# Kernel optimization log

Hardware: AMD Instinct MI355X
Metric: run time of the kernel (lower is better)

Reference implementation:

```python
import jax, jax.numpy as jnp
import numpy as np

NUM_STEPS = 5  # DVF2DDF(num_steps=5)


def _warp(vol, ddf, mode):
    """MONAI Warp: sample vol at (voxel index + ddf), align_corners=True, zeros padding.
    vol: [N,C,D,H,W]; ddf: [N,3,D,H,W] (channels = d,h,w displacement)."""
    N, C, D, H, W = vol.shape
    gd, gh, gw = jnp.meshgrid(jnp.arange(D, dtype=ddf.dtype),
                              jnp.arange(H, dtype=ddf.dtype),
                              jnp.arange(W, dtype=ddf.dtype), indexing='ij')
    cd = gd + ddf[:, 0]  # [N,D,H,W] absolute sample coords
    ch = gh + ddf[:, 1]
    cw = gw + ddf[:, 2]
    vol_flat = vol.reshape(N, C, D * H * W)

    def gather(di, hi, wi, valid):
        dc = jnp.clip(di, 0, D - 1)
        hc = jnp.clip(hi, 0, H - 1)
        wc = jnp.clip(wi, 0, W - 1)
        flat = ((dc * H + hc) * W + wc).reshape(N, 1, -1)
        v = jnp.take_along_axis(vol_flat, flat, axis=2).reshape(N, C, D, H, W)
        return v * valid[:, None]

    def in_bounds(di, hi, wi):
        return ((di >= 0) & (di < D) & (hi >= 0) & (hi < H)
                & (wi >= 0) & (wi < W)).astype(vol.dtype)

    if mode == 'nearest':
        di = jnp.round(cd).astype(jnp.int32)
        hi = jnp.round(ch).astype(jnp.int32)
        wi = jnp.round(cw).astype(jnp.int32)
        return gather(di, hi, wi, in_bounds(di, hi, wi))

    # trilinear ('bilinear' in grid_sample naming)
    d0 = jnp.floor(cd); h0 = jnp.floor(ch); w0 = jnp.floor(cw)
    fd = cd - d0; fh = ch - h0; fw = cw - w0
    d0i = d0.astype(jnp.int32); h0i = h0.astype(jnp.int32); w0i = w0.astype(jnp.int32)
    out = jnp.zeros_like(vol)
    for dd in (0, 1):
        for dh in (0, 1):
            for dw in (0, 1):
                di = d0i + dd; hi = h0i + dh; wi = w0i + dw
                wgt = ((fd if dd else 1 - fd)
                       * (fh if dh else 1 - fh)
                       * (fw if dw else 1 - fw))
                out = out + gather(di, hi, wi, in_bounds(di, hi, wi)) * wgt[:, None]
    return out


def _dvf2ddf(dvf, num_steps=NUM_STEPS):
    """Scaling-and-squaring integration of a stationary velocity field (MONAI DVF2DDF)."""
    ddf = dvf / (2 ** num_steps)
    for _ in range(num_steps):
        ddf = ddf + _warp(ddf, ddf, 'bilinear')
    return ddf


def setup_inputs() -> dict:
    key = jax.random.key(0)
    ks = jax.random.split(key, 6)
    D = H = W = 160
    return {
        "dvf0": jax.random.normal(ks[0], (1, 3, D, H, W), jnp.float32),
        "dvf1": jax.random.normal(ks[1], (1, 3, D, H, W), jnp.float32),
        "image": jax.random.normal(ks[2], (1, 1, D, H, W), jnp.float32),
        "cavity": jax.random.randint(ks[3], (1, 1, D, H, W), 0, 5, jnp.int32),
        "coronary": jax.random.randint(ks[4], (1, 1, D, H, W), 0, 3, jnp.int32),
        "w": jax.random.uniform(ks[5], (), jnp.float32),
    }


def reference(dvf0, dvf1, image, cavity, coronary, w):
    # linear blend of the two neighbouring phase DVFs
    dvf = dvf0 * (1 - w) + dvf1 * w
    ddf = _dvf2ddf(dvf)
    img_warped = _warp(image, ddf, 'bilinear')
    # labels are concatenated along batch and warped with nearest, ddf repeated
    labels = jnp.concatenate([cavity, coronary], axis=0).astype(jnp.float32)  # [2,1,D,H,W]
    lab_warped = _warp(labels, jnp.tile(ddf, (2, 1, 1, 1, 1)), 'nearest')
    cav_warped = lab_warped[0][None].astype(jnp.uint8)
    cor_warped = lab_warped[1][None].astype(jnp.uint8)
    return img_warped, cav_warped, cor_warped, ddf
```

## Files before the change

kernel.cpp:

```cpp
#include <hip/hip_runtime.h>

#define DD 160
#define HH 160
#define WW 160
#define PL (HH*WW)
#define S (DD*PL)

__device__ __forceinline__ float fmul(float a, float b){ return __fmul_rn(a,b); }
__device__ __forceinline__ float fadd(float a, float b){ return __fadd_rn(a,b); }
__device__ __forceinline__ float fsub(float a, float b){ return __fsub_rn(a,b); }

__device__ __forceinline__ void dma16(const float* g, float* l) {
    __builtin_amdgcn_global_load_lds(
        (const __attribute__((address_space(1))) unsigned int*)g,
        (__attribute__((address_space(3))) unsigned int*)l,
        16, 0, 0);
}


template<int H>
__global__ __launch_bounds__(256) void warp_step(const float* __restrict__ in,
                                                 float* __restrict__ out) {
    constexpr int RZ = 4 + 2 * H;
    constexpr int RY = 8 + 2 * H;
    constexpr int ROWS = RZ * RY;
    constexpr int NCH4 = ROWS * 10;
    constexpr int CHF  = ROWS * 40;
    __shared__ __align__(16) float smem[3 * CHF];

    int b  = (blockIdx.x & 7) * 500 + (blockIdx.x >> 3);
    int ix = b % 5;
    int r  = b / 5;
    int iy = r % 20;
    int iz = r / 20;
    int x0 = ix << 5, y0 = iy << 3, z0 = iz << 2;
    int xs4 = x0 - 4, ys = y0 - H, zs = z0 - H;

    int tid = threadIdx.x;
    for (int c = tid; c < NCH4; c += 256) {
        int row = c / 10;
        int col = (c - row * 10) << 2;
        int rz  = row / RY;
        int ry  = row - rz * RY;
        int cz = min(max(zs + rz, 0), DD - 1);
        int cy = min(max(ys + ry, 0), HH - 1);
        int q  = min(max((cz * HH + cy) * WW + xs4 + col, 0), S - 4);
        dma16(in + q,         smem + (c << 2));
        dma16(in + S + q,     smem + CHF + (c << 2));
        dma16(in + 2 * S + q, smem + 2 * CHF + (c << 2));
    }
    __syncthreads();

    int lane = tid & 63, wid = tid >> 6;
    int x = x0 | (lane & 31);
    int y = y0 | (wid << 1) | (lane >> 5);
    int lx = x - xs4;
    int ly = y - ys;

    for (int j = 0; j < 4; ++j) {
        int z = z0 + j;
        int p = (z * HH + y) * WW + x;
        int lc = ((j + H) * RY + ly) * 40 + lx;
        float vd = smem[lc], vh = smem[CHF + lc], vw = smem[2 * CHF + lc];

        float cd = fadd((float)z, vd);
        float ch = fadd((float)y, vh);
        float cw = fadd((float)x, vw);

        float d0 = floorf(cd), h0 = floorf(ch), w0 = floorf(cw);
        float fd = fsub(cd, d0), fh = fsub(ch, h0), fw = fsub(cw, w0);
        float gd = fsub(1.0f, fd), gh = fsub(1.0f, fh), gw = fsub(1.0f, fw);
        int d0i = (int)d0, h0i = (int)h0, w0i = (int)w0;

        int rd = d0i - zs, rh = h0i - ys, rw = w0i - xs4;
        bool ok = ((unsigned)rd < (unsigned)(RZ - 1))
                & ((unsigned)rh < (unsigned)(RY - 1))
                & ((unsigned)rw < 39u);

        float r0, r1, r2;
        if (ok) {
            bool vA0 = (d0i >= 0), vA1 = (d0i + 1 < DD);
            bool vB0 = (h0i >= 0), vB1 = (h0i + 1 < HH);
            bool vC0 = (w0i >= 0), vC1 = (w0i + 1 < WW);
            float wt[8];
            #pragma unroll
            for (int t = 0; t < 8; ++t) {
                int dd = t >> 2, dh = (t >> 1) & 1, dw = t & 1;
                bool valid = (dd ? vA1 : vA0) & (dh ? vB1 : vB0) & (dw ? vC1 : vC0);
                float wgt = fmul(fmul(dd ? fd : gd, dh ? fh : gh), dw ? fw : gw);
                wt[t] = valid ? wgt : 0.0f;
            }
            int l0 = (rd * RY + rh) * 40 + rw;
            const int off[8] = { 0, 1, 40, 41,
                                 RY * 40, RY * 40 + 1, (RY + 1) * 40, (RY + 1) * 40 + 1 };
            float acc0 = 0.0f, acc1 = 0.0f, acc2 = 0.0f;
            #pragma unroll
            for (int t = 0; t < 8; ++t) {
                int li = l0 + off[t];
                acc0 = fadd(acc0, fmul(smem[li], wt[t]));
                acc1 = fadd(acc1, fmul(smem[CHF + li], wt[t]));
                acc2 = fadd(acc2, fmul(smem[2 * CHF + li], wt[t]));
            }
            r0 = fadd(vd, acc0);
            r1 = fadd(vh, acc1);
            r2 = fadd(vw, acc2);
        } else {
            int   qa[8];
            float wt[8];
            #pragma unroll
            for (int t = 0; t < 8; ++t) {
                int dd = t >> 2, dh = (t >> 1) & 1, dw = t & 1;
                int di = d0i + dd, hi = h0i + dh, wi = w0i + dw;
                bool valid = (di >= 0) & (di < DD) & (hi >= 0) & (hi < HH)
                           & (wi >= 0) & (wi < WW);
                float wgt = fmul(fmul(dd ? fd : gd, dh ? fh : gh), dw ? fw : gw);
                wt[t] = valid ? wgt : 0.0f;
                int dc = min(max(di, 0), DD - 1);
                int hc = min(max(hi, 0), HH - 1);
                int wc = min(max(wi, 0), WW - 1);
                qa[t] = (dc * HH + hc) * WW + wc;
            }
            float acc0 = 0.0f, acc1 = 0.0f, acc2 = 0.0f;
            #pragma unroll
            for (int t = 0; t < 8; ++t) {
                acc0 = fadd(acc0, fmul(in[qa[t]], wt[t]));
                acc1 = fadd(acc1, fmul(in[S + qa[t]], wt[t]));
                acc2 = fadd(acc2, fmul(in[2 * S + qa[t]], wt[t]));
            }
            r0 = fadd(vd, acc0);
            r1 = fadd(vh, acc1);
            r2 = fadd(vw, acc2);
        }

        out[p] = r0; out[S + p] = r1; out[2 * S + p] = r2;
    }
}

__global__ __launch_bounds__(256) void fused_init_s1(const float* __restrict__ dvf0,
                                                     const float* __restrict__ dvf1,
                                                     const float* __restrict__ wp,
                                                     float* __restrict__ out) {
    constexpr int H = 1, RZ = 6, RY = 10, ROWS = 60, NCH4 = 600, CHF = 2400;
    __shared__ __align__(16) float smem[3 * CHF];
    float w = wp[0];
    float onew = fsub(1.0f, w);

    int b  = (blockIdx.x & 7) * 500 + (blockIdx.x >> 3);
    int ix = b % 5;
    int r  = b / 5;
    int iy = r % 20;
    int iz = r / 20;
    int x0 = ix << 5, y0 = iy << 3, z0 = iz << 2;
    int xs4 = x0 - 4, ys = y0 - H, zs = z0 - H;

    int tid = threadIdx.x;
    for (int c = tid; c < NCH4; c += 256) {
        int row = c / 10;
        int col = (c - row * 10) << 2;
        int rz  = row / RY;
        int ry  = row - rz * RY;
        int cz = min(max(zs + rz, 0), DD - 1);
        int cy = min(max(ys + ry, 0), HH - 1);
        int q  = min(max((cz * HH + cy) * WW + xs4 + col, 0), S - 4);
        #pragma unroll
        for (int ch = 0; ch < 3; ++ch) {
            float A[4], B[4], O[4];
            *(float4*)A = *(const float4*)(dvf0 + (size_t)ch * S + q);
            *(float4*)B = *(const float4*)(dvf1 + (size_t)ch * S + q);
            #pragma unroll
            for (int k = 0; k < 4; ++k)
                O[k] = fmul(fadd(fmul(A[k], onew), fmul(B[k], w)), 0.03125f);
            *(float4*)&smem[ch * CHF + row * 40 + col] = *(float4*)O;
        }
    }
    __syncthreads();

    int lane = tid & 63, wid = tid >> 6;
    int x = x0 | (lane & 31);
    int y = y0 | (wid << 1) | (lane >> 5);
    int lx = x - xs4;
    int ly = y - ys;

    for (int j = 0; j < 4; ++j) {
        int z = z0 + j;
        int p = (z * HH + y) * WW + x;
        int lc = ((j + H) * RY + ly) * 40 + lx;
        float vd = smem[lc], vh = smem[CHF + lc], vw = smem[2 * CHF + lc];

        float cd = fadd((float)z, vd);
        float ch = fadd((float)y, vh);
        float cw = fadd((float)x, vw);

        float d0 = floorf(cd), h0 = floorf(ch), w0 = floorf(cw);
        float fd = fsub(cd, d0), fh = fsub(ch, h0), fw = fsub(cw, w0);
        float gd = fsub(1.0f, fd), gh = fsub(1.0f, fh), gw = fsub(1.0f, fw);
        int d0i = (int)d0, h0i = (int)h0, w0i = (int)w0;

        int rd = d0i - zs, rh = h0i - ys, rw = w0i - xs4;
        bool ok = ((unsigned)rd < (unsigned)(RZ - 1))
                & ((unsigned)rh < (unsigned)(RY - 1))
                & ((unsigned)rw < 39u);

        float r0, r1, r2;
        if (ok) {
            bool vA0 = (d0i >= 0), vA1 = (d0i + 1 < DD);
            bool vB0 = (h0i >= 0), vB1 = (h0i + 1 < HH);
            bool vC0 = (w0i >= 0), vC1 = (w0i + 1 < WW);
            float wt[8];
            #pragma unroll
            for (int t = 0; t < 8; ++t) {
                int dd = t >> 2, dh = (t >> 1) & 1, dw = t & 1;
                bool valid = (dd ? vA1 : vA0) & (dh ? vB1 : vB0) & (dw ? vC1 : vC0);
                float wgt = fmul(fmul(dd ? fd : gd, dh ? fh : gh), dw ? fw : gw);
                wt[t] = valid ? wgt : 0.0f;
            }
            int l0 = (rd * RY + rh) * 40 + rw;
            const int off[8] = { 0, 1, 40, 41,
                                 RY * 40, RY * 40 + 1, (RY + 1) * 40, (RY + 1) * 40 + 1 };
            float acc0 = 0.0f, acc1 = 0.0f, acc2 = 0.0f;
            #pragma unroll
            for (int t = 0; t < 8; ++t) {
                int li = l0 + off[t];
                acc0 = fadd(acc0, fmul(smem[li], wt[t]));
                acc1 = fadd(acc1, fmul(smem[CHF + li], wt[t]));
                acc2 = fadd(acc2, fmul(smem[2 * CHF + li], wt[t]));
            }
            r0 = fadd(vd, acc0);
            r1 = fadd(vh, acc1);
            r2 = fadd(vw, acc2);
        } else {
            int   qa[8];
            float wt[8];
            #pragma unroll
            for (int t = 0; t < 8; ++t) {
                int dd = t >> 2, dh = (t >> 1) & 1, dw = t & 1;
                int di = d0i + dd, hi = h0i + dh, wi = w0i + dw;
                bool valid = (di >= 0) & (di < DD) & (hi >= 0) & (hi < HH)
                           & (wi >= 0) & (wi < WW);
                float wgt = fmul(fmul(dd ? fd : gd, dh ? fh : gh), dw ? fw : gw);
                wt[t] = valid ? wgt : 0.0f;
                int dc = min(max(di, 0), DD - 1);
                int hc = min(max(hi, 0), HH - 1);
                int wc = min(max(wi, 0), WW - 1);
                qa[t] = (dc * HH + hc) * WW + wc;
            }
            float acc0 = 0.0f, acc1 = 0.0f, acc2 = 0.0f;
            #pragma unroll
            for (int t = 0; t < 8; ++t) {
                float ga = fmul(fadd(fmul(dvf0[qa[t]], onew), fmul(dvf1[qa[t]], w)), 0.03125f);
                float gb = fmul(fadd(fmul(dvf0[S + qa[t]], onew), fmul(dvf1[S + qa[t]], w)), 0.03125f);
                float gc = fmul(fadd(fmul(dvf0[2 * S + qa[t]], onew), fmul(dvf1[2 * S + qa[t]], w)), 0.03125f);
                acc0 = fadd(acc0, fmul(ga, wt[t]));
                acc1 = fadd(acc1, fmul(gb, wt[t]));
                acc2 = fadd(acc2, fmul(gc, wt[t]));
            }
            r0 = fadd(vd, acc0);
            r1 = fadd(vh, acc1);
            r2 = fadd(vw, acc2);
        }

        out[p] = r0; out[S + p] = r1; out[2 * S + p] = r2;
    }
}

__global__ __launch_bounds__(256) void final_phased(const float* __restrict__ ddf4,
                                                    const float* __restrict__ image,
                                                    const int* __restrict__ cav,
                                                    const int* __restrict__ cor,
                                                    float* __restrict__ outImg,
                                                    float* __restrict__ outDdf) {
    constexpr int RZ = 8, RY = 12, ROWS = 96, NCH4 = 960, CHF = 3840;
    __shared__ __align__(16) float smem[2 * CHF];

    int b  = (blockIdx.x & 7) * 500 + (blockIdx.x >> 3);
    int ix = b % 5;
    int r  = b / 5;
    int iy = r % 20;
    int iz = r / 20;
    int x0 = ix << 5, y0 = iy << 3, z0 = iz << 2;
    int xs4 = x0 - 4, ys = y0 - 2, zs = z0 - 2;

    int tid = threadIdx.x;
    int lane = tid & 63, wid = tid >> 6;
    int x = x0 | (lane & 31);
    int y = y0 | (wid << 1) | (lane >> 5);
    int p0 = (z0 * HH + y) * WW + x;

    #pragma unroll 1
    for (int cc = tid; cc < NCH4; cc += 256) {
        int row = cc / 10;
        int col = (cc - row * 10) << 2;
        int rz  = row / RY;
        int ry  = row - rz * RY;
        int cz = min(max(zs + rz, 0), DD - 1);
        int cy = min(max(ys + ry, 0), HH - 1);
        int q  = min(max((cz * HH + cy) * WW + xs4 + col, 0), S - 4);
        dma16(ddf4 + q, smem + (cc << 2));
    }

    float ctd[4], cth[4], ctw[4];
    #pragma unroll
    for (int j = 0; j < 4; ++j) {
        ctd[j] = ddf4[p0 + j * PL];
        cth[j] = ddf4[S + p0 + j * PL];
        ctw[j] = ddf4[2 * S + p0 + j * PL];
    }

    float wt[4][8];
    int   l0[4];
    int   okm = 0;
    const int off[8] = { 0, 1, 40, 41,
                         RY * 40, RY * 40 + 1, (RY + 1) * 40, (RY + 1) * 40 + 1 };
    #pragma unroll
    for (int j = 0; j < 4; ++j) {
        int z = z0 + j;
        float cd = fadd((float)z, ctd[j]);
        float ch = fadd((float)y, cth[j]);
        float cw = fadd((float)x, ctw[j]);
        float d0 = floorf(cd), h0 = floorf(ch), w0 = floorf(cw);
        float fd = fsub(cd, d0), fh = fsub(ch, h0), fw = fsub(cw, w0);
        float gd = fsub(1.0f, fd), gh = fsub(1.0f, fh), gw = fsub(1.0f, fw);
        int d0i = (int)d0, h0i = (int)h0, w0i = (int)w0;

        bool vA0 = (d0i >= 0), vA1 = (d0i + 1 < DD);
        bool vB0 = (h0i >= 0), vB1 = (h0i + 1 < HH);
        bool vC0 = (w0i >= 0), vC1 = (w0i + 1 < WW);
        #pragma unroll
        for (int t = 0; t < 8; ++t) {
            int dd = t >> 2, dh = (t >> 1) & 1, dw = t & 1;
            bool valid = (dd ? vA1 : vA0) & (dh ? vB1 : vB0) & (dw ? vC1 : vC0);
            float wgt = fmul(fmul(dd ? fd : gd, dh ? fh : gh), dw ? fw : gw);
            wt[j][t] = valid ? wgt : 0.0f;
        }
        int rd = d0i - zs, rh = h0i - ys, rw = w0i - xs4;
        bool ok = ((unsigned)rd < (unsigned)(RZ - 1))
                & ((unsigned)rh < (unsigned)(RY - 1))
                & ((unsigned)rw < 39u);
        l0[j] = (rd * RY + rh) * 40 + rw;
        okm |= (ok ? 1 : 0) << j;
    }

    float fb[3][4];
    if (okm != 15) {
        #pragma unroll
        for (int j = 0; j < 4; ++j) {
            if (!((okm >> j) & 1)) {
                int z = z0 + j;
                float cd = fadd((float)z, ctd[j]);
                float ch = fadd((float)y, cth[j]);
                float cw = fadd((float)x, ctw[j]);
                float d0 = floorf(cd), h0 = floorf(ch), w0 = floorf(cw);
                float fd = fsub(cd, d0), fh = fsub(ch, h0), fw = fsub(cw, w0);
                float gd = fsub(1.0f, fd), gh = fsub(1.0f, fh), gw = fsub(1.0f, fw);
                int d0i = (int)d0, h0i = (int)h0, w0i = (int)w0;
                int   qa[8];
                float wtf[8];
                #pragma unroll
                for (int t = 0; t < 8; ++t) {
                    int dd = t >> 2, dh = (t >> 1) & 1, dw = t & 1;
                    int di = d0i + dd, hi = h0i + dh, wi = w0i + dw;
                    bool valid = (di >= 0) & (di < DD) & (hi >= 0) & (hi < HH)
                               & (wi >= 0) & (wi < WW);
                    float wgt = fmul(fmul(dd ? fd : gd, dh ? fh : gh), dw ? fw : gw);
                    wtf[t] = valid ? wgt : 0.0f;
                    int dc = min(max(di, 0), DD - 1);
                    int hc = min(max(hi, 0), HH - 1);
                    int wc = min(max(wi, 0), WW - 1);
                    qa[t] = (dc * HH + hc) * WW + wc;
                }
                float a0 = 0.0f, a1 = 0.0f, a2 = 0.0f;
                #pragma unroll
                for (int t = 0; t < 8; ++t) {
                    a0 = fadd(a0, fmul(ddf4[qa[t]], wtf[t]));
                    a1 = fadd(a1, fmul(ddf4[S + qa[t]], wtf[t]));
                    a2 = fadd(a2, fmul(ddf4[2 * S + qa[t]], wtf[t]));
                }
                fb[0][j] = a0; fb[1][j] = a1; fb[2][j] = a2;
            }
        }
    }

    __syncthreads();

    float rr[3][4];
    #pragma unroll
    for (int c = 0; c < 3; ++c) {
        if (c < 2) {
            const float* src = ddf4 + (size_t)(c + 1) * S;
            float* buf = smem + ((c + 1) & 1) * CHF;
            #pragma unroll 1
            for (int cc = tid; cc < NCH4; cc += 256) {
                int row = cc / 10;
                int col = (cc - row * 10) << 2;
                int rz  = row / RY;
                int ry  = row - rz * RY;
                int cz = min(max(zs + rz, 0), DD - 1);
                int cy = min(max(ys + ry, 0), HH - 1);
                int q  = min(max((cz * HH + cy) * WW + xs4 + col, 0), S - 4);
                dma16(src + q, buf + (cc << 2));
            }
        }
        const float* g = smem + (c & 1) * CHF;
        #pragma unroll
        for (int j = 0; j < 4; ++j) {
            float ctr = (c == 0) ? ctd[j] : (c == 1) ? cth[j] : ctw[j];
            float acc = 0.0f;
            if ((okm >> j) & 1) {
                #pragma unroll
                for (int t = 0; t < 8; ++t)
                    acc = fadd(acc, fmul(g[l0[j] + off[t]], wt[j][t]));
                rr[c][j] = fadd(ctr, acc);
            } else {
                rr[c][j] = fadd(ctr, fb[c][j]);
            }
            outDdf[(size_t)c * S + p0 + j * PL] = rr[c][j];
        }
        __syncthreads();
    }

    #pragma unroll
    for (int j = 0; j < 4; ++j) {
        int z = z0 + j;
        int p = p0 + j * PL;
        float r0 = rr[0][j], r1 = rr[1][j], r2 = rr[2][j];

        float cd2 = fadd((float)z, r0);
        float ch2 = fadd((float)y, r1);
        float cw2 = fadd((float)x, r2);
        float d02 = floorf(cd2), h02 = floorf(ch2), w02 = floorf(cw2);
        float fd2 = fsub(cd2, d02), fh2 = fsub(ch2, h02), fw2 = fsub(cw2, w02);
        float gd2 = fsub(1.0f, fd2), gh2 = fsub(1.0f, fh2), gw2 = fsub(1.0f, fw2);
        int d2i = (int)d02, h2i = (int)h02, w2i = (int)w02;

        bool fast = ((unsigned)d2i < (unsigned)(DD - 1))
                  & ((unsigned)h2i < (unsigned)(HH - 1))
                  & ((unsigned)w2i < (unsigned)(WW - 1));
        if (fast) {
            const float* bp0 = image + (d2i * HH + h2i) * WW + w2i;
            const float* bp1 = bp0 + PL;
            float g[8];
            g[0] = bp0[0];      g[1] = bp0[1];
            g[2] = bp0[WW];     g[3] = bp0[WW + 1];
            g[4] = bp1[0];      g[5] = bp1[1];
            g[6] = bp1[WW];     g[7] = bp1[WW + 1];
            float w00 = fmul(gd2, gh2), w01 = fmul(gd2, fh2);
            float w10 = fmul(fd2, gh2), w11 = fmul(fd2, fh2);
            float wtf[8] = { fmul(w00, gw2), fmul(w00, fw2), fmul(w01, gw2), fmul(w01, fw2),
                             fmul(w10, gw2), fmul(w10, fw2), fmul(w11, gw2), fmul(w11, fw2) };
            float a = 0.0f;
            #pragma unroll
            for (int t = 0; t < 8; ++t) a = fadd(a, fmul(g[t], wtf[t]));
            outImg[p] = a;

            int di = (int)rintf(cd2), hi = (int)rintf(ch2), wi = (int)rintf(cw2);
            int q = (di * HH + hi) * WW + wi;
            outImg[S + p]     = (float)cav[q];
            outImg[2 * S + p] = (float)cor[q];
        } else {
            int   qb[8];
            float wtf[8];
            #pragma unroll
            for (int t = 0; t < 8; ++t) {
                int dd = t >> 2, dh = (t >> 1) & 1, dw = t & 1;
                int di = d2i + dd, hi = h2i + dh, wi = w2i + dw;
                bool valid = (di >= 0) & (di < DD) & (hi >= 0) & (hi < HH)
                           & (wi >= 0) & (wi < WW);
                float wgt = fmul(fmul(dd ? fd2 : gd2, dh ? fh2 : gh2), dw ? fw2 : gw2);
                wtf[t] = valid ? wgt : 0.0f;
                int dc = min(max(di, 0), DD - 1);
                int hc = min(max(hi, 0), HH - 1);
                int wc = min(max(wi, 0), WW - 1);
                qb[t] = (dc * HH + hc) * WW + wc;
            }
            float a = 0.0f;
            #pragma unroll
            for (int t = 0; t < 8; ++t) a = fadd(a, fmul(image[qb[t]], wtf[t]));
            outImg[p] = a;

            int di = (int)rintf(cd2), hi = (int)rintf(ch2), wi = (int)rintf(cw2);
            bool valid = (di >= 0) & (di < DD) & (hi >= 0) & (hi < HH)
                       & (wi >= 0) & (wi < WW);
            int dc = min(max(di, 0), DD - 1);
            int hc = min(max(hi, 0), HH - 1);
            int wc = min(max(wi, 0), WW - 1);
            int q = (dc * HH + hc) * WW + wc;
            outImg[S + p]     = valid ? (float)cav[q] : 0.0f;
            outImg[2 * S + p] = valid ? (float)cor[q] : 0.0f;
        }
    }
}

__global__ __launch_bounds__(256) void warp_flat(const float* __restrict__ in,
                                                 float* __restrict__ out) {
    int b  = (blockIdx.x & 7) * 1000 + (blockIdx.x >> 3);
    int ix = b % 5;
    int r  = b / 5;
    int iy = r % 20;
    int iz = r / 20;
    int lane = threadIdx.x & 63, wid = threadIdx.x >> 6;
    int x  = (ix << 5) | (lane & 31);
    int y  = (iy << 3) | (wid << 1) | (lane >> 5);
    int z0 = iz << 1;
    int p0 = (z0 * HH + y) * WW + x;

    #pragma unroll
    for (int j = 0; j < 2; ++j) {
        int z = z0 + j;
        int p = p0 + j * PL;
        float vd = in[p], vh = in[S + p], vw = in[2 * S + p];
        float cd = fadd((float)z, vd);
        float ch = fadd((float)y, vh);
        float cw = fadd((float)x, vw);

        float d0 = floorf(cd), h0 = floorf(ch), w0 = floorf(cw);
        float fd = fsub(cd, d0), fh = fsub(ch, h0), fw = fsub(cw, w0);
        float gd = fsub(1.0f, fd), gh = fsub(1.0f, fh), gw = fsub(1.0f, fw);
        int d0i = (int)d0, h0i = (int)h0, w0i = (int)w0;

        int   qa[8];
        float wt[8];
        #pragma unroll
        for (int t = 0; t < 8; ++t) {
            int dd = t >> 2, dh = (t >> 1) & 1, dw = t & 1;
            int di = d0i + dd, hi = h0i + dh, wi = w0i + dw;
            bool valid = (di >= 0) & (di < DD) & (hi >= 0) & (hi < HH)
                       & (wi >= 0) & (wi < WW);
            float wgt = fmul(fmul(dd ? fd : gd, dh ? fh : gh), dw ? fw : gw);
            wt[t] = valid ? wgt : 0.0f;
            int dc = min(max(di, 0), DD - 1);
            int hc = min(max(hi, 0), HH - 1);
            int wc = min(max(wi, 0), WW - 1);
            qa[t] = (dc * HH + hc) * WW + wc;
        }
        float acc0 = 0.0f, acc1 = 0.0f, acc2 = 0.0f;
        #pragma unroll
        for (int t = 0; t < 8; ++t) {
            acc0 = fadd(acc0, fmul(in[qa[t]], wt[t]));
            acc1 = fadd(acc1, fmul(in[S + qa[t]], wt[t]));
            acc2 = fadd(acc2, fmul(in[2 * S + qa[t]], wt[t]));
        }
        out[p]         = fadd(vd, acc0);
        out[S + p]     = fadd(vh, acc1);
        out[2 * S + p] = fadd(vw, acc2);
    }
}

__global__ __launch_bounds__(256) void final_kernel(const float* __restrict__ ddf,
                                                    const float* __restrict__ image,
                                                    const int* __restrict__ cav,
                                                    const int* __restrict__ cor,
                                                    float* __restrict__ out) {
    int b  = (blockIdx.x & 7) * 1000 + (blockIdx.x >> 3);
    int ix = b % 5;
    int r  = b / 5;
    int iy = r % 20;
    int iz = r / 20;
    int lane = threadIdx.x & 63, wid = threadIdx.x >> 6;
    int x  = (ix << 5) | (lane & 31);
    int y  = (iy << 3) | (wid << 1) | (lane >> 5);
    int z0 = iz << 1;
    int p0 = (z0 * HH + y) * WW + x;

    #pragma unroll
    for (int j = 0; j < 2; ++j) {
        int z = z0 + j;
        int p = p0 + j * PL;
        float cd = fadd((float)z, ddf[p]);
        float ch = fadd((float)y, ddf[S + p]);
        float cw = fadd((float)x, ddf[2 * S + p]);

        float d0 = floorf(cd), h0 = floorf(ch), w0 = floorf(cw);
        float fd = fsub(cd, d0), fh = fsub(ch, h0), fw = fsub(cw, w0);
        float gd = fsub(1.0f, fd), gh = fsub(1.0f, fh), gw = fsub(1.0f, fw);
        int d0i = (int)d0, h0i = (int)h0, w0i = (int)w0;

        int   qa[8];
        float wt[8];
        #pragma unroll
        for (int t = 0; t < 8; ++t) {
            int dd = t >> 2, dh = (t >> 1) & 1, dw = t & 1;
            int di = d0i + dd, hi = h0i + dh, wi = w0i + dw;
            bool valid = (di >= 0) & (di < DD) & (hi >= 0) & (hi < HH)
                       & (wi >= 0) & (wi < WW);
            float wgt = fmul(fmul(dd ? fd : gd, dh ? fh : gh), dw ? fw : gw);
            wt[t] = valid ? wgt : 0.0f;
            int dc = min(max(di, 0), DD - 1);
            int hc = min(max(hi, 0), HH - 1);
            int wc = min(max(wi, 0), WW - 1);
            qa[t] = (dc * HH + hc) * WW + wc;
        }
        float acc = 0.0f;
        #pragma unroll
        for (int t = 0; t < 8; ++t) acc = fadd(acc, fmul(image[qa[t]], wt[t]));
        out[p] = acc;

        int di = (int)rintf(cd), hi = (int)rintf(ch), wi = (int)rintf(cw);
        bool valid = (di >= 0) & (di < DD) & (hi >= 0) & (hi < HH)
                   & (wi >= 0) & (wi < WW);
        int dc = min(max(di, 0), DD - 1);
        int hc = min(max(hi, 0), HH - 1);
        int wc = min(max(wi, 0), WW - 1);
        int q = (dc * HH + hc) * WW + wc;
        out[S + p]     = valid ? (float)cav[q] : 0.0f;
        out[2 * S + p] = valid ? (float)cor[q] : 0.0f;
    }
}

extern "C" void kernel_launch(void* const* d_in, const int* in_sizes, int n_in,
                              void* d_out, int out_size, void* d_ws, size_t ws_size,
                              hipStream_t stream) {
    const float* dvf0   = (const float*)d_in[0];
    const float* dvf1   = (const float*)d_in[1];
    const float* image  = (const float*)d_in[2];
    const int*   cav    = (const int*)d_in[3];
    const int*   cor    = (const int*)d_in[4];
    const float* w      = (const float*)d_in[5];

    float* out  = (float*)d_out;
    float* bufA = out;
    float* bufB = out + (size_t)3 * S;
    float* bufC = (float*)d_ws;
    bool useWs = (d_ws != nullptr) && (ws_size >= (size_t)3 * S * sizeof(float));

    fused_init_s1<<<4000, 256, 0, stream>>>(dvf0, dvf1, w, bufB);
    warp_step<1><<<4000, 256, 0, stream>>>(bufB, bufA);
    warp_step<1><<<4000, 256, 0, stream>>>(bufA, bufB);
    if (useWs) {
        warp_step<1><<<4000, 256, 0, stream>>>(bufB, bufC);
        final_phased<<<4000, 256, 0, stream>>>(bufC, image, cav, cor, bufA, bufB);
    } else {
        warp_step<1><<<4000, 256, 0, stream>>>(bufB, bufA);
        warp_flat<<<8000, 256, 0, stream>>>(bufA, bufB);
        final_kernel<<<8000, 256, 0, stream>>>(bufB, image, cav, cor, bufA);
    }
}
```

Baseline: 351.1 us.

## Overlap LDS halo DMA with center loads and weight computation in warp_step

```diff
diff --git a/kernel.cpp b/kernel.cpp
--- a/kernel.cpp
+++ b/kernel.cpp
@@ -49,89 +49,118 @@
         dma16(in + S + q,     smem + CHF + (c << 2));
         dma16(in + 2 * S + q, smem + 2 * CHF + (c << 2));
     }
-    __syncthreads();
 
     int lane = tid & 63, wid = tid >> 6;
     int x = x0 | (lane & 31);
     int y = y0 | (wid << 1) | (lane >> 5);
-    int lx = x - xs4;
-    int ly = y - ys;
-
+    int p0 = (z0 * HH + y) * WW + x;
+
+    float ctd[4], cth[4], ctw[4];
+    #pragma unroll
+    for (int j = 0; j < 4; ++j) {
+        ctd[j] = in[p0 + j * PL];
+        cth[j] = in[S + p0 + j * PL];
+        ctw[j] = in[2 * S + p0 + j * PL];
+    }
+
+    float wt[4][8];
+    int   l0[4];
+    int   okm = 0;
+    const int off[8] = { 0, 1, 40, 41,
+                         RY * 40, RY * 40 + 1, (RY + 1) * 40, (RY + 1) * 40 + 1 };
+    #pragma unroll
     for (int j = 0; j < 4; ++j) {
         int z = z0 + j;
-        int p = (z * HH + y) * WW + x;
-        int lc = ((j + H) * RY + ly) * 40 + lx;
-        float vd = smem[lc], vh = smem[CHF + lc], vw = smem[2 * CHF + lc];
-
-        float cd = fadd((float)z, vd);
-        float ch = fadd((float)y, vh);
-        float cw = fadd((float)x, vw);
-
+        float cd = fadd((float)z, ctd[j]);
+        float ch = fadd((float)y, cth[j]);
+        float cw = fadd((float)x, ctw[j]);
         float d0 = floorf(cd), h0 = floorf(ch), w0 = floorf(cw);
         float fd = fsub(cd, d0), fh = fsub(ch, h0), fw = fsub(cw, w0);
         float gd = fsub(1.0f, fd), gh = fsub(1.0f, fh), gw = fsub(1.0f, fw);
         int d0i = (int)d0, h0i = (int)h0, w0i = (int)w0;
 
+        bool vA0 = (d0i >= 0), vA1 = (d0i + 1 < DD);
+        bool vB0 = (h0i >= 0), vB1 = (h0i + 1 < HH);
+        bool vC0 = (w0i >= 0), vC1 = (w0i + 1 < WW);
+        #pragma unroll
+        for (int t = 0; t < 8; ++t) {
+            int dd = t >> 2, dh = (t >> 1) & 1, dw = t & 1;
+            bool valid = (dd ? vA1 : vA0) & (dh ? vB1 : vB0) & (dw ? vC1 : vC0);
+            float wgt = fmul(fmul(dd ? fd : gd, dh ? fh : gh), dw ? fw : gw);
+            wt[j][t] = valid ? wgt : 0.0f;
+        }
         int rd = d0i - zs, rh = h0i - ys, rw = w0i - xs4;
         bool ok = ((unsigned)rd < (unsigned)(RZ - 1))
                 & ((unsigned)rh < (unsigned)(RY - 1))
                 & ((unsigned)rw < 39u);
-
+        l0[j] = (rd * RY + rh) * 40 + rw;
+        okm |= (ok ? 1 : 0) << j;
+    }
+
+    float fb[3][4];
+    if (okm != 15) {
+        #pragma unroll
+        for (int j = 0; j < 4; ++j) {
+            if (!((okm >> j) & 1)) {
+                int z = z0 + j;
+                float cd = fadd((float)z, ctd[j]);
+                float ch = fadd((float)y, cth[j]);
+                float cw = fadd((float)x, ctw[j]);
+                float d0 = floorf(cd), h0 = floorf(ch), w0 = floorf(cw);
+                float fd = fsub(cd, d0), fh = fsub(ch, h0), fw = fsub(cw, w0);
+                float gd = fsub(1.0f, fd), gh = fsub(1.0f, fh), gw = fsub(1.0f, fw);
+                int d0i = (int)d0, h0i = (int)h0, w0i = (int)w0;
+                int   qa[8];
+                float wtf[8];
+                #pragma unroll
+                for (int t = 0; t < 8; ++t) {
+                    int dd = t >> 2, dh = (t >> 1) & 1, dw = t & 1;
+                    int di = d0i + dd, hi = h0i + dh, wi = w0i + dw;
+                    bool valid = (di >= 0) & (di < DD) & (hi >= 0) & (hi < HH)
+                               & (wi >= 0) & (wi < WW);
+                    float wgt = fmul(fmul(dd ? fd : gd, dh ? fh : gh), dw ? fw : gw);
+                    wtf[t] = valid ? wgt : 0.0f;
+                    int dc = min(max(di, 0), DD - 1);
+                    int hc = min(max(hi, 0), HH - 1);
+                    int wc = min(max(wi, 0), WW - 1);
+                    qa[t] = (dc * HH + hc) * WW + wc;
+                }
+                float a0 = 0.0f, a1 = 0.0f, a2 = 0.0f;
+                #pragma unroll
+                for (int t = 0; t < 8; ++t) {
+                    a0 = fadd(a0, fmul(in[qa[t]], wtf[t]));
+                    a1 = fadd(a1, fmul(in[S + qa[t]], wtf[t]));
+                    a2 = fadd(a2, fmul(in[2 * S + qa[t]], wtf[t]));
+                }
+                fb[0][j] = a0; fb[1][j] = a1; fb[2][j] = a2;
+            }
+        }
+    }
+
+    __syncthreads();
+
+    #pragma unroll
+    for (int j = 0; j < 4; ++j) {
+        int p = p0 + j * PL;
         float r0, r1, r2;
-        if (ok) {
-            bool vA0 = (d0i >= 0), vA1 = (d0i + 1 < DD);
-            bool vB0 = (h0i >= 0), vB1 = (h0i + 1 < HH);
-            bool vC0 = (w0i >= 0), vC1 = (w0i + 1 < WW);
-            float wt[8];
+        if ((okm >> j) & 1) {
+            int lb = l0[j];
+            float acc0 = 0.0f, acc1 = 0.0f, acc2 = 0.0f;
             #pragma unroll
             for (int t = 0; t < 8; ++t) {
-                int dd = t >> 2, dh = (t >> 1) & 1, dw = t & 1;
-                bool valid = (dd ? vA1 : vA0) & (dh ? vB1 : vB0) & (dw ? vC1 : vC0);
-                float wgt = fmul(fmul(dd ? fd : gd, dh ? fh : gh), dw ? fw : gw);
-                wt[t] = valid ? wgt : 0.0f;
-            }
-            int l0 = (rd * RY + rh) * 40 + rw;
-            const int off[8] = { 0, 1, 40, 41,
-                                 RY * 40, RY * 40 + 1, (RY + 1) * 40, (RY + 1) * 40 + 1 };
-            float acc0 = 0.0f, acc1 = 0.0f, acc2 = 0.0f;
-            #pragma unroll
-            for (int t = 0; t < 8; ++t) {
-                int li = l0 + off[t];
-                acc0 = fadd(acc0, fmul(smem[li], wt[t]));
-                acc1 = fadd(acc1, fmul(smem[CHF + li], wt[t]));
-                acc2 = fadd(acc2, fmul(smem[2 * CHF + li], wt[t]));
-            }
-            r0 = fadd(vd, acc0);
-            r1 = fadd(vh, acc1);
-            r2 = fadd(vw, acc2);
+                int li = lb + off[t];
+                acc0 = fadd(acc0, fmul(smem[li], wt[j][t]));
+                acc1 = fadd(acc1, fmul(smem[CHF + li], wt[j][t]));
+                acc2 = fadd(acc2, fmul(smem[2 * CHF + li], wt[j][t]));
+            }
+            r0 = fadd(ctd[j], acc0);
+            r1 = fadd(cth[j], acc1);
+            r2 = fadd(ctw[j], acc2);
         } else {
-            int   qa[8];
-            float wt[8];
-            #pragma unroll
-            for (int t = 0; t < 8; ++t) {
-                int dd = t >> 2, dh = (t >> 1) & 1, dw = t & 1;
-                int di = d0i + dd, hi = h0i + dh, wi = w0i + dw;
-                bool valid = (di >= 0) & (di < DD) & (hi >= 0) & (hi < HH)
-                           & (wi >= 0) & (wi < WW);
-                float wgt = fmul(fmul(dd ? fd : gd, dh ? fh : gh), dw ? fw : gw);
-                wt[t] = valid ? wgt : 0.0f;
-                int dc = min(max(di, 0), DD - 1);
-                int hc = min(max(hi, 0), HH - 1);
-                int wc = min(max(wi, 0), WW - 1);
-                qa[t] = (dc * HH + hc) * WW + wc;
-            }
-            float acc0 = 0.0f, acc1 = 0.0f, acc2 = 0.0f;
-            #pragma unroll
-            for (int t = 0; t < 8; ++t) {
-                acc0 = fadd(acc0, fmul(in[qa[t]], wt[t]));
-                acc1 = fadd(acc1, fmul(in[S + qa[t]], wt[t]));
-                acc2 = fadd(acc2, fmul(in[2 * S + qa[t]], wt[t]));
-            }
-            r0 = fadd(vd, acc0);
-            r1 = fadd(vh, acc1);
-            r2 = fadd(vw, acc2);
-        }
-
+            r0 = fadd(ctd[j], fb[0][j]);
+            r1 = fadd(cth[j], fb[1][j]);
+            r2 = fadd(ctw[j], fb[2][j]);
+        }
         out[p] = r0; out[S + p] = r1; out[2 * S + p] = r2;
     }
 }
```

Result: no change. 356.2 us (+1.4%).
